# Kernel optimization log

Hardware: AMD Instinct MI355X
Metric: run time of the kernel (lower is better)

The kernel has to match this reference:

```python
import jax, jax.numpy as jnp
import numpy as np
from jax import lax

T, D_IN, N = 8192, 1024, 1024


def setup_inputs() -> dict:
    key = jax.random.key(0)
    ks = jax.random.split(key, 8)
    s = 0.1  # truncated_normal stddev in original
    return {
        "x": jax.random.normal(ks[0], (T, D_IN), jnp.float32),
        # input projections (FullConnectLayer weights + biases)
        "Wx": jax.random.normal(ks[1], (D_IN, N), jnp.float32) * s,
        "bx": jnp.zeros((N,), jnp.float32),
        "Wu": jax.random.normal(ks[2], (D_IN, N), jnp.float32) * s,
        "bu": jnp.zeros((N,), jnp.float32),
        "Wr": jax.random.normal(ks[3], (D_IN, N), jnp.float32) * s,
        "br": jnp.zeros((N,), jnp.float32),
        # recurrent weights/biases
        "hW": jax.random.normal(ks[4], (N, N), jnp.float32) * s,
        "hUW": jax.random.normal(ks[5], (N, N), jnp.float32) * s,
        "hRW": jax.random.normal(ks[6], (N, N), jnp.float32) * s,
        "hB": jnp.zeros((N,), jnp.float32),
        "hUB": jnp.zeros((N,), jnp.float32),
        "hRB": jnp.zeros((N,), jnp.float32),
        # initial hidden state h (tf.Variable zeros [1, nNodes])
        "h0": jnp.zeros((1, N), jnp.float32),
    }


def reference(x, Wx, bx, Wu, bu, Wr, br, hW, hUW, hRW, hB, hUB, hRB, h0):
    # Precompute input-side gate projections for all timesteps (as original
    # does: xTransform/xUpdates/xResets are built once on the full sequence).
    xT = x @ Wx + bx  # [T, N] candidate input
    xU = x @ Wu + bu  # [T, N] update gate input
    xR = x @ Wr + br  # [T, N] reset gate input

    def step(h, xs):  # h: [N]
        xt, xu, xr = xs
        u = jax.nn.sigmoid(xu + h @ hUW + hUB)
        r = jax.nn.sigmoid(xr + h @ hRW + hRB)
        hc = jnp.tanh(xt + (r * h) @ hW + hB)
        # NOTE: faithful to original bug: (1-u)*hc + u*hc == hc
        h_new = (1.0 - u) * hc + u * hc
        return h_new, h_new

    _, hs = lax.scan(step, h0[0], (xT, xU, xR))
    return hs  # [T, N] == hStates.concat() since each state is [1, N]
```

## Files before the change

### kernel.cpp

```cpp
#include <hip/hip_runtime.h>
#include <hip/hip_bf16.h>
#include <math.h>

#define T_STEPS 8192
#define NN      1024
#define KWG     32
#define RT      512

__device__ __forceinline__ float fast_sigmoid(float z) {
    z = fminf(fmaxf(z, -30.f), 30.f);
    return 1.f / (1.f + __expf(-z));
}
__device__ __forceinline__ float fast_tanh(float x) {
    x = fminf(fmaxf(x, -9.f), 9.f);
    const float e = __expf(2.f * x);
    return (e - 1.f) / (e + 1.f);
}

__global__ __launch_bounds__(256) void gemm_bias(
    const float* __restrict__ A, const float* __restrict__ W,
    const float* __restrict__ bias, float* __restrict__ C)
{
    const int bn = blockIdx.x;
    const int bm = blockIdx.y;
    const int tid = threadIdx.x;

    __shared__ __align__(16) float As[16][68];
    __shared__ __align__(16) float Bs[16][68];

    const int row0 = bm * 64, col0 = bn * 64;
    const int tm = (tid >> 4) << 2;
    const int tn = (tid & 15) << 2;

    float acc[4][4] = {};

    for (int k0 = 0; k0 < 1024; k0 += 16) {
        {
            const int m = tid >> 2, kq = (tid & 3) << 2;
            const float4 v = *reinterpret_cast<const float4*>(&A[(size_t)(row0 + m) * 1024 + k0 + kq]);
            As[kq + 0][m] = v.x; As[kq + 1][m] = v.y; As[kq + 2][m] = v.z; As[kq + 3][m] = v.w;
            const int kk = tid >> 4, nq = (tid & 15) << 2;
            *reinterpret_cast<float4*>(&Bs[kk][nq]) =
                *reinterpret_cast<const float4*>(&W[(size_t)(k0 + kk) * 1024 + col0 + nq]);
        }
        __syncthreads();
#pragma unroll
        for (int k = 0; k < 16; ++k) {
            const float4 a4 = *reinterpret_cast<const float4*>(&As[k][tm]);
            const float4 b4 = *reinterpret_cast<const float4*>(&Bs[k][tn]);
            const float a[4] = {a4.x, a4.y, a4.z, a4.w};
            const float b[4] = {b4.x, b4.y, b4.z, b4.w};
#pragma unroll
            for (int i = 0; i < 4; ++i)
#pragma unroll
                for (int j = 0; j < 4; ++j) acc[i][j] += a[i] * b[j];
        }
        __syncthreads();
    }
#pragma unroll
    for (int i = 0; i < 4; ++i)
#pragma unroll
        for (int j = 0; j < 4; ++j)
            C[(size_t)(row0 + tm + i) * 1024 + col0 + tn + j] = acc[i][j] + bias[col0 + tn + j];
}

__global__ __launch_bounds__(RT, 2) void gru_rec(
    const float* __restrict__ xT, const float* __restrict__ xR,
    const float* __restrict__ hRW, const float* __restrict__ hW,
    const float* __restrict__ hRB, const float* __restrict__ hB,
    const float* __restrict__ h0, float* __restrict__ out,
    unsigned long long* __restrict__ slots)
{
    const int g = blockIdx.x;
    const int tid = threadIdx.x;
    const int lane = tid & 63;
    const int wave = tid >> 6;

    __shared__ __align__(16) float hsh[1088];
    __shared__ __align__(16) float rh[32];

    const int j = (wave << 2) | (lane >> 4);
    const int c = lane & 15;
    const bool leader = (c == 0);

    float w1[64];
#pragma unroll
    for (int k = 0; k < 64; ++k)
        w1[k] = hRW[(size_t)(c * 64 + k) * NN + g * 32 + j];

    const int n0 = tid, n1 = tid + RT;
    const int pi0 = n0 + (n0 >> 6) * 4, pi1 = n1 + (n1 >> 6) * 4;
    float w2a[32], w2b[32];
#pragma unroll
    for (int k = 0; k < 32; ++k) {
        w2a[k] = hW[(size_t)(g * 32 + k) * NN + n0];
        w2b[k] = hW[(size_t)(g * 32 + k) * NN + n1];
    }
    const float hB0 = hB[n0], hB1 = hB[n1];
    const int mj = g * 32 + j;
    const int pij = mj + (mj >> 6) * 4;
    const float hRBj = leader ? hRB[mj] : 0.f;
    const bool own0 = ((n0 >> 5) == g), own1 = ((n1 >> 5) == g);

    hsh[pi0] = h0[n0];
    hsh[pi1] = h0[n1];
    __syncthreads();

    float hp0 = 0.f, hp1 = 0.f;
    unsigned long long pA0 = 0, pA1 = 0, pB0 = 0, pB1 = 0;
    unsigned long long tgA = 0, tgB = 0;
    const float SC = 1048576.f, ISC = 1.f / 1048576.f;

#define GRU_STEP(T_, SL_, PV0_, PV1_, TG_) do { \
    const float xt0 = xT[(size_t)(T_) * NN + n0]; \
    const float xt1 = xT[(size_t)(T_) * NN + n1]; \
    float xr = 0.f; \
    if (leader) xr = xR[(size_t)(T_) * NN + mj]; \
    if ((T_) > 0) {   \
        if (own0) out[(size_t)((T_) - 1) * NN + n0] = hp0; \
        if (own1) out[(size_t)((T_) - 1) * NN + n1] = hp1; \
    } \
    float a0 = 0.f, a1 = 0.f, a2 = 0.f, a3 = 0.f; \
    _Pragma("unroll") \
    for (int k = 0; k < 64; k += 4) { \
        const float4 hv = *reinterpret_cast<const float4*>(&hsh[c * 68 + k]); \
        a0 += hv.x * w1[k + 0]; a1 += hv.y * w1[k + 1]; \
        a2 += hv.z * w1[k + 2]; a3 += hv.w * w1[k + 3]; \
    } \
    float s = (a0 + a1) + (a2 + a3); \
    s += __shfl_xor(s, 1); s += __shfl_xor(s, 2); \
    s += __shfl_xor(s, 4); s += __shfl_xor(s, 8); \
    if (leader) rh[j] = fast_sigmoid(xr + hRBj + s) * hsh[pij]; \
    __syncthreads(); \
    float b0 = 0.f, b1 = 0.f, d0 = 0.f, d1 = 0.f; \
    _Pragma("unroll") \
    for (int k = 0; k < 32; k += 2) { \
        const float2 rv = *reinterpret_cast<const float2*>(&rh[k]); \
        b0 += rv.x * w2a[k]; b1 += rv.y * w2a[k + 1]; \
        d0 += rv.x * w2b[k]; d1 += rv.y * w2b[k + 1]; \
    } \
    const unsigned long long q0 = (1ULL << 38) + \
        (unsigned long long)(long long)llrintf((b0 + b1) * SC); \
    const unsigned long long q1 = (1ULL << 38) + \
        (unsigned long long)(long long)llrintf((d0 + d1) * SC); \
    __hip_atomic_fetch_add(&(SL_)[n0], q0, __ATOMIC_RELAXED, __HIP_MEMORY_SCOPE_AGENT); \
    __hip_atomic_fetch_add(&(SL_)[n1], q1, __ATOMIC_RELAXED, __HIP_MEMORY_SCOPE_AGENT); \
    TG_ += (unsigned long long)KWG << 38; \
    const long long thr = (long long)TG_ - (1LL << 36); \
    unsigned long long v0 = 0, v1 = 0; \
    bool f0 = false, f1 = false; \
    do { \
        if (!f0) { v0 = __hip_atomic_load(&(SL_)[n0], __ATOMIC_RELAXED, __HIP_MEMORY_SCOPE_AGENT); \
                   f0 = ((long long)v0 >= thr); } \
        if (!f1) { v1 = __hip_atomic_load(&(SL_)[n1], __ATOMIC_RELAXED, __HIP_MEMORY_SCOPE_AGENT); \
                   f1 = ((long long)v1 >= thr); } \
    } while (!(f0 && f1)); \
    const float s0 = (float)(long long)(v0 - PV0_ - ((unsigned long long)KWG << 38)) * ISC; \
    const float s1 = (float)(long long)(v1 - PV1_ - ((unsigned long long)KWG << 38)) * ISC; \
    PV0_ = v0; PV1_ = v1; \
    hp0 = fast_tanh(xt0 + s0 + hB0); \
    hp1 = fast_tanh(xt1 + s1 + hB1); \
    hsh[pi0] = hp0; hsh[pi1] = hp1; \
    __syncthreads(); \
} while (0)

    for (int t = 0; t < T_STEPS; t += 2) {
        GRU_STEP(t,     slots,      pA0, pA1, tgA);
        GRU_STEP(t + 1, slots + NN, pB0, pB1, tgB);
    }
#undef GRU_STEP
    if (own0) out[(size_t)(T_STEPS - 1) * NN + n0] = hp0;
    if (own1) out[(size_t)(T_STEPS - 1) * NN + n1] = hp1;
}

extern "C" void kernel_launch(void* const* d_in, const int* in_sizes, int n_in,
                              void* d_out, int out_size, void* d_ws, size_t ws_size,
                              hipStream_t stream) {
    const float* x   = (const float*)d_in[0];
    const float* Wx  = (const float*)d_in[1];
    const float* bx  = (const float*)d_in[2];
    const float* Wr  = (const float*)d_in[5];
    const float* br  = (const float*)d_in[6];
    const float* hW  = (const float*)d_in[7];
    const float* hRW = (const float*)d_in[9];
    const float* hB  = (const float*)d_in[10];
    const float* hRB = (const float*)d_in[12];
    const float* h0  = (const float*)d_in[13];
    float* out = (float*)d_out;

    char* ws = (char*)d_ws;
    float* xT = (float*)(ws);
    float* xR = (float*)(ws + 33554432);
    unsigned long long* slots = (unsigned long long*)(ws + 67108864);

    hipMemsetAsync(slots, 0, 2 * NN * sizeof(unsigned long long), stream);

    gemm_bias<<<dim3(16, 128), 256, 0, stream>>>(x, Wx, bx, xT);
    gemm_bias<<<dim3(16, 128), 256, 0, stream>>>(x, Wr, br, xR);

    gru_rec<<<dim3(KWG), RT, 0, stream>>>(xT, xR, hRW, hW, hRB, hB, h0,
                                          out, slots);
}
```

Baseline: 33.07 ms.

## Replace fixed-point atomic-add reduction with tagged partial stores and owner-reduced broadcast

The cross-block reduction of the candidate matvec no longer uses fixed-point atomic adds into shared slots. Each block now stores tagged float partials to a per-block buffer. The owning block gathers the 32 partials for its rows, applies tanh, writes the output, and broadcasts the tagged new h through a second buffer that every block polls. This removes atomic read-modify-write contention and fixed-point quantization. In exchange it adds a second global handshake per step and lowers the occupancy hint to one block per CU.

```diff
diff --git a/kernel.cpp b/kernel.cpp
--- a/kernel.cpp
+++ b/kernel.cpp
@@ -64,12 +64,13 @@
             C[(size_t)(row0 + tm + i) * 1024 + col0 + tn + j] = acc[i][j] + bias[col0 + tn + j];
 }
 
-__global__ __launch_bounds__(RT, 2) void gru_rec(
+__global__ __launch_bounds__(RT, 1) void gru_rec(
     const float* __restrict__ xT, const float* __restrict__ xR,
     const float* __restrict__ hRW, const float* __restrict__ hW,
     const float* __restrict__ hRB, const float* __restrict__ hB,
     const float* __restrict__ h0, float* __restrict__ out,
-    unsigned long long* __restrict__ slots)
+    unsigned long long* __restrict__ P,
+    unsigned long long* __restrict__ hbc)
 {
     const int g = blockIdx.x;
     const int tid = threadIdx.x;
@@ -81,8 +82,7 @@
 
     const int j = (wave << 2) | (lane >> 4);
     const int c = lane & 15;
-    const bool leader = (c == 0);
-
+    const bool leader1 = (c == 0);
     float w1[64];
 #pragma unroll
     for (int k = 0; k < 64; ++k)
@@ -96,81 +96,95 @@
         w2a[k] = hW[(size_t)(g * 32 + k) * NN + n0];
         w2b[k] = hW[(size_t)(g * 32 + k) * NN + n1];
     }
-    const float hB0 = hB[n0], hB1 = hB[n1];
+
+    const int jj = tid >> 4, cc = tid & 15;
+    const bool eleader = (cc == 0);
+    const int mjj = g * 32 + jj;
+    const float hBo = hB[mjj];
+
     const int mj = g * 32 + j;
     const int pij = mj + (mj >> 6) * 4;
-    const float hRBj = leader ? hRB[mj] : 0.f;
-    const bool own0 = ((n0 >> 5) == g), own1 = ((n1 >> 5) == g);
+    const float hRBj = hRB[mj];
 
     hsh[pi0] = h0[n0];
     hsh[pi1] = h0[n1];
     __syncthreads();
 
-    float hp0 = 0.f, hp1 = 0.f;
-    unsigned long long pA0 = 0, pA1 = 0, pB0 = 0, pB1 = 0;
-    unsigned long long tgA = 0, tgB = 0;
-    const float SC = 1048576.f, ISC = 1.f / 1048576.f;
-
-#define GRU_STEP(T_, SL_, PV0_, PV1_, TG_) do { \
-    const float xt0 = xT[(size_t)(T_) * NN + n0]; \
-    const float xt1 = xT[(size_t)(T_) * NN + n1]; \
-    float xr = 0.f; \
-    if (leader) xr = xR[(size_t)(T_) * NN + mj]; \
-    if ((T_) > 0) {   \
-        if (own0) out[(size_t)((T_) - 1) * NN + n0] = hp0; \
-        if (own1) out[(size_t)((T_) - 1) * NN + n1] = hp1; \
-    } \
-    float a0 = 0.f, a1 = 0.f, a2 = 0.f, a3 = 0.f; \
-    _Pragma("unroll") \
-    for (int k = 0; k < 64; k += 4) { \
-        const float4 hv = *reinterpret_cast<const float4*>(&hsh[c * 68 + k]); \
-        a0 += hv.x * w1[k + 0]; a1 += hv.y * w1[k + 1]; \
-        a2 += hv.z * w1[k + 2]; a3 += hv.w * w1[k + 3]; \
-    } \
-    float s = (a0 + a1) + (a2 + a3); \
-    s += __shfl_xor(s, 1); s += __shfl_xor(s, 2); \
-    s += __shfl_xor(s, 4); s += __shfl_xor(s, 8); \
-    if (leader) rh[j] = fast_sigmoid(xr + hRBj + s) * hsh[pij]; \
-    __syncthreads(); \
-    float b0 = 0.f, b1 = 0.f, d0 = 0.f, d1 = 0.f; \
-    _Pragma("unroll") \
-    for (int k = 0; k < 32; k += 2) { \
-        const float2 rv = *reinterpret_cast<const float2*>(&rh[k]); \
-        b0 += rv.x * w2a[k]; b1 += rv.y * w2a[k + 1]; \
-        d0 += rv.x * w2b[k]; d1 += rv.y * w2b[k + 1]; \
-    } \
-    const unsigned long long q0 = (1ULL << 38) + \
-        (unsigned long long)(long long)llrintf((b0 + b1) * SC); \
-    const unsigned long long q1 = (1ULL << 38) + \
-        (unsigned long long)(long long)llrintf((d0 + d1) * SC); \
-    __hip_atomic_fetch_add(&(SL_)[n0], q0, __ATOMIC_RELAXED, __HIP_MEMORY_SCOPE_AGENT); \
-    __hip_atomic_fetch_add(&(SL_)[n1], q1, __ATOMIC_RELAXED, __HIP_MEMORY_SCOPE_AGENT); \
-    TG_ += (unsigned long long)KWG << 38; \
-    const long long thr = (long long)TG_ - (1LL << 36); \
-    unsigned long long v0 = 0, v1 = 0; \
-    bool f0 = false, f1 = false; \
-    do { \
-        if (!f0) { v0 = __hip_atomic_load(&(SL_)[n0], __ATOMIC_RELAXED, __HIP_MEMORY_SCOPE_AGENT); \
-                   f0 = ((long long)v0 >= thr); } \
-        if (!f1) { v1 = __hip_atomic_load(&(SL_)[n1], __ATOMIC_RELAXED, __HIP_MEMORY_SCOPE_AGENT); \
-                   f1 = ((long long)v1 >= thr); } \
-    } while (!(f0 && f1)); \
-    const float s0 = (float)(long long)(v0 - PV0_ - ((unsigned long long)KWG << 38)) * ISC; \
-    const float s1 = (float)(long long)(v1 - PV1_ - ((unsigned long long)KWG << 38)) * ISC; \
-    PV0_ = v0; PV1_ = v1; \
-    hp0 = fast_tanh(xt0 + s0 + hB0); \
-    hp1 = fast_tanh(xt1 + s1 + hB1); \
-    hsh[pi0] = hp0; hsh[pi1] = hp1; \
-    __syncthreads(); \
-} while (0)
-
-    for (int t = 0; t < T_STEPS; t += 2) {
-        GRU_STEP(t,     slots,      pA0, pA1, tgA);
-        GRU_STEP(t + 1, slots + NN, pB0, pB1, tgB);
+    for (int t = 0; t < T_STEPS; ++t) {
+        const unsigned tag = (unsigned)(t + 1);
+        unsigned long long* __restrict__ Pb = P + (size_t)(t & 1) * KWG * NN;
+        unsigned long long* __restrict__ Hb = hbc + (size_t)(t & 1) * NN;
+
+        float xr = 0.f, xto = 0.f;
+        if (leader1) xr  = xR[(size_t)t * NN + mj];
+        if (eleader) xto = xT[(size_t)t * NN + mjj];
+
+        float a0 = 0.f, a1 = 0.f, a2 = 0.f, a3 = 0.f;
+#pragma unroll
+        for (int k = 0; k < 64; k += 4) {
+            const float4 hv = *reinterpret_cast<const float4*>(&hsh[c * 68 + k]);
+            a0 += hv.x * w1[k + 0]; a1 += hv.y * w1[k + 1];
+            a2 += hv.z * w1[k + 2]; a3 += hv.w * w1[k + 3];
+        }
+        float s = (a0 + a1) + (a2 + a3);
+        s += __shfl_xor(s, 1); s += __shfl_xor(s, 2);
+        s += __shfl_xor(s, 4); s += __shfl_xor(s, 8);
+        if (leader1) rh[j] = fast_sigmoid(xr + hRBj + s) * hsh[pij];
+        __syncthreads();
+
+        float b0 = 0.f, b1 = 0.f, d0 = 0.f, d1 = 0.f;
+#pragma unroll
+        for (int k = 0; k < 32; k += 2) {
+            const float2 rv = *reinterpret_cast<const float2*>(&rh[k]);
+            b0 += rv.x * w2a[k]; b1 += rv.y * w2a[k + 1];
+            d0 += rv.x * w2b[k]; d1 += rv.y * w2b[k + 1];
+        }
+        const unsigned long long q0 =
+            ((unsigned long long)tag << 32) | (unsigned)__float_as_uint(b0 + b1);
+        const unsigned long long q1 =
+            ((unsigned long long)tag << 32) | (unsigned)__float_as_uint(d0 + d1);
+        __hip_atomic_store(&Pb[(size_t)g * NN + n0], q0, __ATOMIC_RELAXED, __HIP_MEMORY_SCOPE_AGENT);
+        __hip_atomic_store(&Pb[(size_t)g * NN + n1], q1, __ATOMIC_RELAXED, __HIP_MEMORY_SCOPE_AGENT);
+
+        {
+            unsigned long long va = 0, vb = 0;
+            bool fa = false, fb = false;
+            do {
+                if (!fa) { va = __hip_atomic_load(&Pb[(size_t)cc * NN + mjj],
+                             __ATOMIC_RELAXED, __HIP_MEMORY_SCOPE_AGENT);
+                           fa = ((unsigned)(va >> 32) == tag); }
+                if (!fb) { vb = __hip_atomic_load(&Pb[(size_t)(cc + 16) * NN + mjj],
+                             __ATOMIC_RELAXED, __HIP_MEMORY_SCOPE_AGENT);
+                           fb = ((unsigned)(vb >> 32) == tag); }
+            } while (!(fa && fb));
+            float s2 = __uint_as_float((unsigned)va) + __uint_as_float((unsigned)vb);
+            s2 += __shfl_xor(s2, 1); s2 += __shfl_xor(s2, 2);
+            s2 += __shfl_xor(s2, 4); s2 += __shfl_xor(s2, 8);
+            if (eleader) {
+                const float hn = fast_tanh(xto + s2 + hBo);
+                out[(size_t)t * NN + mjj] = hn;
+                __hip_atomic_store(&Hb[mjj],
+                    ((unsigned long long)tag << 32) | (unsigned)__float_as_uint(hn),
+                    __ATOMIC_RELAXED, __HIP_MEMORY_SCOPE_AGENT);
+            }
+        }
+
+        {
+            unsigned long long ua = 0, ub = 0;
+            bool fa = false, fb = false;
+            do {
+                if (!fa) { ua = __hip_atomic_load(&Hb[n0], __ATOMIC_RELAXED,
+                             __HIP_MEMORY_SCOPE_AGENT);
+                           fa = ((unsigned)(ua >> 32) == tag); }
+                if (!fb) { ub = __hip_atomic_load(&Hb[n1], __ATOMIC_RELAXED,
+                             __HIP_MEMORY_SCOPE_AGENT);
+                           fb = ((unsigned)(ub >> 32) == tag); }
+            } while (!(fa && fb));
+            hsh[pi0] = __uint_as_float((unsigned)ua);
+            hsh[pi1] = __uint_as_float((unsigned)ub);
+        }
+        __syncthreads();
     }
-#undef GRU_STEP
-    if (own0) out[(size_t)(T_STEPS - 1) * NN + n0] = hp0;
-    if (own1) out[(size_t)(T_STEPS - 1) * NN + n1] = hp1;
 }
 
 extern "C" void kernel_launch(void* const* d_in, const int* in_sizes, int n_in,
@@ -191,13 +205,14 @@
     char* ws = (char*)d_ws;
     float* xT = (float*)(ws);
     float* xR = (float*)(ws + 33554432);
-    unsigned long long* slots = (unsigned long long*)(ws + 67108864);
-
-    hipMemsetAsync(slots, 0, 2 * NN * sizeof(unsigned long long), stream);
+    unsigned long long* P   = (unsigned long long*)(ws + 67108864);
+    unsigned long long* hbc = (unsigned long long*)(ws + 67108864 + 524288);
+
+    hipMemsetAsync(P, 0, (2 * KWG * NN + 2 * NN) * sizeof(unsigned long long), stream);
 
     gemm_bias<<<dim3(16, 128), 256, 0, stream>>>(x, Wx, bx, xT);
     gemm_bias<<<dim3(16, 128), 256, 0, stream>>>(x, Wr, br, xR);
 
     gru_rec<<<dim3(KWG), RT, 0, stream>>>(xT, xR, hRW, hW, hRB, hB, h0,
-                                          out, slots);
-}
+                                          out, P, hbc);
+}
```

Result: no change. 32.73 ms (-1.0%).
